# Optimization experiments

Hardware: AMD Instinct MI355X
Metric: run time of the kernel (lower is better)

The kernel has to match this reference:

```python
import jax, jax.numpy as jnp
import numpy as np

SEQ_LEN, N_VARS, N_SKILLS, D_IN = 120, 9, 32, 1
BATCH = 32768


def setup_inputs() -> dict:
    key = jax.random.key(0)
    ks = jax.random.split(key, 8)
    H, D = N_SKILLS, D_IN
    s = 1.0 / np.sqrt(H)  # torch LSTMCell init scale
    return {
        "x": jax.random.normal(ks[0], (BATCH, N_VARS * SEQ_LEN), dtype=jnp.float32),
        # nn.LSTMCell params (gate order i,f,g,o)
        "W_ih": jax.random.uniform(ks[1], (4 * H, D), jnp.float32, -s, s),
        "W_hh": jax.random.uniform(ks[2], (4 * H, H), jnp.float32, -s, s),
        "b_ih": jax.random.uniform(ks[3], (4 * H,), jnp.float32, -s, s),
        "b_hh": jax.random.uniform(ks[4], (4 * H,), jnp.float32, -s, s),
        # contextual gate params: cg_w Linear(D,H,bias=False), cg_u Linear(H,H)
        "cg_w": jax.random.uniform(ks[5], (H, D), jnp.float32, -s, s),
        "cg_u": jax.random.uniform(ks[6], (H, H), jnp.float32, -s, s),
        "cg_b": jax.random.uniform(ks[7], (H,), jnp.float32, -s, s),
    }


def reference(x, W_ih, W_hh, b_ih, b_hh, cg_w, cg_u, cg_b):
    B = x.shape[0]
    H = N_SKILLS
    # [B, V*T] -> fold the 9 independent variable-sequences into the batch dim
    # (the same cell weights are shared across vars), then scan over time.
    xs = x.reshape(B * N_VARS, SEQ_LEN, D_IN)
    xs = jnp.moveaxis(xs, 1, 0)  # [T, B*V, D_IN]

    def step(carry, xt):
        h, c = carry  # each [B*V, H]
        gates = xt @ W_ih.T + b_ih + h @ W_hh.T + b_hh  # [B*V, 4H]
        i, f, g, o = jnp.split(gates, 4, axis=-1)
        i = jax.nn.sigmoid(i)
        f = jax.nn.sigmoid(f)
        g = jnp.tanh(g)
        c_new = f * c + i * g
        # contextual gate uses the *previous* h
        cg = jax.nn.sigmoid(xt @ cg_w.T + h @ cg_u.T + cg_b)
        h_new = cg * jnp.tanh(c_new)
        return (h_new, c_new), None

    zeros = jnp.zeros((B * N_VARS, H), dtype=x.dtype)
    (h, _), _ = jax.lax.scan(step, (zeros, zeros), xs)
    # [B*V, H] -> [B, V*H] (variable-major, matching torch.cat over vars)
    return h.reshape(B, N_VARS * H)
```

## Files before the change

### kernel.cpp

```cpp
#include <hip/hip_runtime.h>


#define NV 9
#define TLEN 120
#define HS 32
#define BATCH_ 32768
#define NSEQ (BATCH_ * NV)
#define NBATCH (NSEQ / 16)
#define WPB 4
#define GRID_ (NBATCH / WPB)

#define TCHUNK 60
#define XSTRIDE 20
#define HSTRIDE 36

#define XT_WORDS   (TCHUNK * XSTRIDE)
#define HB_WORDS   (16 * HSTRIDE)
#define XT_OFF     0
#define HB_OFF     (WPB * XT_WORDS)
#define BLO_OFF    (HB_OFF + WPB * HB_WORDS)
#define POOL_WORDS (BLO_OFF + 8 * 64 * 4)

#define LOG2E 1.4426950408889634f
#define TWOL  2.8853900817779268f

typedef __attribute__((ext_vector_type(8))) short bf16x8;
typedef __attribute__((ext_vector_type(4))) float f32x4;
typedef __attribute__((ext_vector_type(4))) unsigned int u32x4;

__device__ __forceinline__ float fast_exp2(float x) { return __builtin_amdgcn_exp2f(x); }
__device__ __forceinline__ float fast_rcp(float x)  { return __builtin_amdgcn_rcpf(x); }
__device__ __forceinline__ unsigned int fbits(float x) { return __builtin_bit_cast(unsigned int, x); }
__device__ __forceinline__ float bcastf(unsigned int x) { return __builtin_bit_cast(float, x); }

__device__ __forceinline__ f32x4 splat4(float x) { f32x4 v = {x, x, x, x}; return v; }
__device__ __forceinline__ f32x4 fma4(f32x4 a, f32x4 b, f32x4 c) {
  return __builtin_elementwise_fma(a, b, c);
}
__device__ __forceinline__ f32x4 exp24(f32x4 v) {
  f32x4 r;
  r[0] = fast_exp2(v[0]); r[1] = fast_exp2(v[1]);
  r[2] = fast_exp2(v[2]); r[3] = fast_exp2(v[3]);
  return r;
}
__device__ __forceinline__ f32x4 rcp4(f32x4 v) {
  f32x4 r;
  r[0] = fast_rcp(v[0]); r[1] = fast_rcp(v[1]);
  r[2] = fast_rcp(v[2]); r[3] = fast_rcp(v[3]);
  return r;
}

__device__ __forceinline__ void lstm_elem(f32x4 ai, f32x4 af, f32x4 ag, f32x4 ac,
                                          f32x4& ct, f32x4& h) {
  const f32x4 one4 = splat4(1.0f);
  f32x4 Ei = exp24(ai), Ef = exp24(af), Eg = exp24(ag), Ea = exp24(ac);
  f32x4 pi_ = Ei + one4, pf_ = Ef + one4, pg_ = Eg + one4, pa_ = Ea + one4;
  f32x4 u   = fma4(Eg, splat4(TWOL), splat4(-TWOL));
  f32x4 P   = pi_ * pg_;
  f32x4 tt  = pf_ * u;
  f32x4 num = fma4(ct, P, tt);
  f32x4 den = pf_ * P;
  ct = num * rcp4(den);
  f32x4 Ec  = exp24(ct);
  h = (one4 - Ec) * rcp4(pa_ * (Ec + one4));
}

__global__ __launch_bounds__(256, 2) void cglstm_kernel(
    const float* __restrict__ x,
    const float* __restrict__ W_ih,
    const float* __restrict__ W_hh,
    const float* __restrict__ b_ih,
    const float* __restrict__ b_hh,
    const float* __restrict__ cg_w,
    const float* __restrict__ cg_u,
    const float* __restrict__ cg_b,
    float* __restrict__ out)
{
  const int lane = threadIdx.x & 63;
  const int wid  = threadIdx.x >> 6;
  const int col  = lane & 15;
  const int quad = lane >> 4;

  __shared__ __align__(16) unsigned int pool[POOL_WORDS];
  float* __restrict__ xTw = (float*)&pool[XT_OFF + wid * XT_WORDS];
  unsigned int* hb = &pool[HB_OFF + wid * HB_WORDS];
  u32x4* blo_t = (u32x4*)&pool[BLO_OFF];

  bf16x8 bhi[8];
  float wx[8], bb[8];
#pragma unroll
  for (int tile = 0; tile < 8; ++tile) {
    const int n = col + (tile & 1) * 16;
    const float sc_ = ((tile >> 1) == 2) ? -TWOL : -LOG2E;
    const float* wrow = (tile < 6) ? (W_hh + (size_t)((tile >> 1) * HS + n) * HS)
                                   : (cg_u + (size_t)n * HS);
    bf16x8 vh, vl;
#pragma unroll
    for (int e = 0; e < 8; ++e) {
      float wv = wrow[quad * 8 + e] * sc_;
      unsigned int wbits = fbits(wv);
      float lo_f = wv - bcastf(wbits & 0xffff0000u);
      vh[e] = (short)(wbits >> 16);
      vl[e] = (short)(fbits(lo_f) >> 16);
    }
    bhi[tile] = vh;
    blo_t[tile * 64 + lane] = __builtin_bit_cast(u32x4, vl);
    if (tile < 6) {
      const int gg = tile >> 1;
      wx[tile] = W_ih[gg * HS + n] * sc_;
      bb[tile] = (b_ih[gg * HS + n] + b_hh[gg * HS + n]) * sc_;
    } else {
      wx[tile] = cg_w[n] * sc_;
      bb[tile] = cg_b[n] * sc_;
    }
  }

  const int p = blockIdx.x * WPB + wid;
  const float4* xb = (const float4*)(x + (size_t)p * 16 * TLEN);

  for (int i = lane; i < 16 * HSTRIDE; i += 64) hb[i] = 0u;
  f32x4 ct0 = splat4(0.f), ct1 = splat4(0.f), h0 = splat4(0.f), h1 = splat4(0.f);

#pragma unroll 1
  for (int chunk = 0; chunk < 2; ++chunk) {
    for (int i = lane; i < 240; i += 64) {
      int s = i / 15;
      int j = i - s * 15;
      float4 v = xb[s * 30 + chunk * 15 + j];
      int t0 = j * 4;
      xTw[(t0 + 0) * XSTRIDE + s] = v.x;
      xTw[(t0 + 1) * XSTRIDE + s] = v.y;
      xTw[(t0 + 2) * XSTRIDE + s] = v.z;
      xTw[(t0 + 3) * XSTRIDE + s] = v.w;
    }

#pragma unroll 1
    for (int tl = 0; tl < TCHUNK; ++tl) {
      f32x4 xt4 = *(const f32x4*)&xTw[tl * XSTRIDE + quad * 4];
      f32x4 acc[8];
#pragma unroll
      for (int tile = 0; tile < 8; ++tile)
        acc[tile] = fma4(splat4(wx[tile]), xt4, splat4(bb[tile]));
      const unsigned int* hrow = &hb[col * HSTRIDE + quad * 8];
      u32x4 wa = *(const u32x4*)hrow;
      u32x4 wz = *(const u32x4*)(hrow + 4);
      u32x4 hi4, lo4;
      hi4[0] = __builtin_amdgcn_perm(wa[1], wa[0], 0x05040100u);
      hi4[1] = __builtin_amdgcn_perm(wa[3], wa[2], 0x05040100u);
      hi4[2] = __builtin_amdgcn_perm(wz[1], wz[0], 0x05040100u);
      hi4[3] = __builtin_amdgcn_perm(wz[3], wz[2], 0x05040100u);
      lo4[0] = __builtin_amdgcn_perm(wa[1], wa[0], 0x07060302u);
      lo4[1] = __builtin_amdgcn_perm(wa[3], wa[2], 0x07060302u);
      lo4[2] = __builtin_amdgcn_perm(wz[1], wz[0], 0x07060302u);
      lo4[3] = __builtin_amdgcn_perm(wz[3], wz[2], 0x07060302u);
      bf16x8 ahi = __builtin_bit_cast(bf16x8, hi4);
      bf16x8 alo = __builtin_bit_cast(bf16x8, lo4);
#pragma unroll
      for (int tile = 0; tile < 8; ++tile) {
        bf16x8 blo_c = __builtin_bit_cast(bf16x8, blo_t[tile * 64 + lane]);
        acc[tile] = __builtin_amdgcn_mfma_f32_16x16x32_bf16(ahi, bhi[tile], acc[tile], 0, 0, 0);
        acc[tile] = __builtin_amdgcn_mfma_f32_16x16x32_bf16(alo, bhi[tile], acc[tile], 0, 0, 0);
        acc[tile] = __builtin_amdgcn_mfma_f32_16x16x32_bf16(ahi, blo_c, acc[tile], 0, 0, 0);
      }
      lstm_elem(acc[0], acc[2], acc[4], acc[6], ct0, h0);
      lstm_elem(acc[1], acc[3], acc[5], acc[7], ct1, h1);
#pragma unroll
      for (int r = 0; r < 4; ++r) {
        unsigned int hbits = fbits(h0[r]);
        float lof = h0[r] - bcastf(hbits & 0xffff0000u);
        hb[(quad * 4 + r) * HSTRIDE + col] =
            __builtin_amdgcn_perm(fbits(lof), hbits, 0x07060302u);
        unsigned int hbits1 = fbits(h1[r]);
        float lof1 = h1[r] - bcastf(hbits1 & 0xffff0000u);
        hb[(quad * 4 + r) * HSTRIDE + col + 16] =
            __builtin_amdgcn_perm(fbits(lof1), hbits1, 0x07060302u);
      }
    }
  }

  float* ob = out + (size_t)p * 16 * HS;
#pragma unroll
  for (int r = 0; r < 4; ++r) {
    ob[(quad * 4 + r) * HS + col]      = h0[r];
    ob[(quad * 4 + r) * HS + col + 16] = h1[r];
  }
}

extern "C" void kernel_launch(void* const* d_in, const int* in_sizes, int n_in,
                              void* d_out, int out_size, void* d_ws, size_t ws_size,
                              hipStream_t stream) {
  const float* x    = (const float*)d_in[0];
  const float* W_ih = (const float*)d_in[1];
  const float* W_hh = (const float*)d_in[2];
  const float* b_ih = (const float*)d_in[3];
  const float* b_hh = (const float*)d_in[4];
  const float* cg_w = (const float*)d_in[5];
  const float* cg_u = (const float*)d_in[6];
  const float* cg_b = (const float*)d_in[7];
  float* out = (float*)d_out;

  dim3 grid(GRID_), block(256);
  hipLaunchKernelGGL(cglstm_kernel, grid, block, 0, stream,
                     x, W_ih, W_hh, b_ih, b_hh, cg_w, cg_u, cg_b, out);
}
```

Baseline: 1.367 ms.

## Pre-transpose x in a separate kernel and stream timesteps from global memory

Adds a transpose kernel that writes x in time-major order per 16-sequence group to the workspace. The LSTM kernel then prefetches the next timestep's inputs straight from global memory instead of staging chunks through LDS. It also keeps the low bf16 weight halves in registers rather than LDS and groups the MFMAs by pass. This removes the in-kernel LDS transpose and cuts LDS use, in exchange for an extra launch, a full write and re-read of x through the workspace, and higher register pressure. The old path is kept as a fallback for when the workspace is too small.

```diff
diff --git a/kernel.cpp b/kernel.cpp
--- a/kernel.cpp
+++ b/kernel.cpp
@@ -10,16 +10,12 @@
 #define WPB 4
 #define GRID_ (NBATCH / WPB)
 
-#define TCHUNK 60
-#define XSTRIDE 20
 #define HSTRIDE 36
-
-#define XT_WORDS   (TCHUNK * XSTRIDE)
+#define WBSTRIDE 20
+
 #define HB_WORDS   (16 * HSTRIDE)
-#define XT_OFF     0
-#define HB_OFF     (WPB * XT_WORDS)
-#define BLO_OFF    (HB_OFF + WPB * HB_WORDS)
-#define POOL_WORDS (BLO_OFF + 8 * 64 * 4)
+#define WB_OFF     (WPB * HB_WORDS)
+#define POOL_WORDS (WB_OFF + 16 * WBSTRIDE)
 
 #define LOG2E 1.4426950408889634f
 #define TWOL  2.8853900817779268f
@@ -65,8 +61,30 @@
   h = (one4 - Ec) * rcp4(pa_ * (Ec + one4));
 }
 
+__global__ __launch_bounds__(256) void xpose_kernel(
+    const float* __restrict__ x, float* __restrict__ xt) {
+  const int p = blockIdx.x;
+  __shared__ float tile[16 * TLEN];
+  const float4* xb = (const float4*)(x + (size_t)p * 16 * TLEN);
+  float4* ob = (float4*)(xt + (size_t)p * 16 * TLEN);
+  for (int i = threadIdx.x; i < 480; i += 256)
+    ((float4*)tile)[i] = xb[i];
+  __syncthreads();
+  for (int i = threadIdx.x; i < 480; i += 256) {
+    int o0 = i * 4;
+    int t  = o0 >> 4;
+    int e  = o0 & 15;
+    float4 v;
+    v.x = tile[(e + 0) * TLEN + t];
+    v.y = tile[(e + 1) * TLEN + t];
+    v.z = tile[(e + 2) * TLEN + t];
+    v.w = tile[(e + 3) * TLEN + t];
+    ob[i] = v;
+  }
+}
+
 __global__ __launch_bounds__(256, 2) void cglstm_kernel(
-    const float* __restrict__ x,
+    const float* __restrict__ xt_ws,
     const float* __restrict__ W_ih,
     const float* __restrict__ W_hh,
     const float* __restrict__ b_ih,
@@ -82,9 +100,134 @@
   const int quad = lane >> 4;
 
   __shared__ __align__(16) unsigned int pool[POOL_WORDS];
-  float* __restrict__ xTw = (float*)&pool[XT_OFF + wid * XT_WORDS];
-  unsigned int* hb = &pool[HB_OFF + wid * HB_WORDS];
-  u32x4* blo_t = (u32x4*)&pool[BLO_OFF];
+  unsigned int* hb = &pool[wid * HB_WORDS];
+  float* wbt = (float*)&pool[WB_OFF];
+
+  bf16x8 bhi[8], blo[8];
+#pragma unroll
+  for (int tile = 0; tile < 8; ++tile) {
+    const int n = col + (tile & 1) * 16;
+    const float sc_ = ((tile >> 1) == 2) ? -TWOL : -LOG2E;
+    const float* wrow = (tile < 6) ? (W_hh + (size_t)((tile >> 1) * HS + n) * HS)
+                                   : (cg_u + (size_t)n * HS);
+    bf16x8 vh, vl;
+#pragma unroll
+    for (int e = 0; e < 8; ++e) {
+      float wv = wrow[quad * 8 + e] * sc_;
+      unsigned int wbits = fbits(wv);
+      float lo_f = wv - bcastf(wbits & 0xffff0000u);
+      vh[e] = (short)(wbits >> 16);
+      vl[e] = (short)(fbits(lo_f) >> 16);
+    }
+    bhi[tile] = vh; blo[tile] = vl;
+    float wxv, bbv;
+    if (tile < 6) {
+      const int gg = tile >> 1;
+      wxv = W_ih[gg * HS + n] * sc_;
+      bbv = (b_ih[gg * HS + n] + b_hh[gg * HS + n]) * sc_;
+    } else {
+      wxv = cg_w[n] * sc_;
+      bbv = cg_b[n] * sc_;
+    }
+    if (quad == 0) {
+      wbt[col * WBSTRIDE + tile]     = wxv;
+      wbt[col * WBSTRIDE + 8 + tile] = bbv;
+    }
+  }
+
+  const int p = blockIdx.x * WPB + wid;
+  const f32x4* xrow = (const f32x4*)(xt_ws + (size_t)p * 16 * TLEN);
+
+  for (int i = lane; i < HB_WORDS / 4; i += 64) ((u32x4*)hb)[i] = u32x4{0,0,0,0};
+  f32x4 ct0 = splat4(0.f), ct1 = splat4(0.f), h0 = splat4(0.f), h1 = splat4(0.f);
+
+  f32x4 xt_cur = xrow[quad];
+
+#pragma unroll 1
+  for (int t = 0; t < TLEN; ++t) {
+    int tn = (t < TLEN - 1) ? (t + 1) : t;
+    f32x4 xt_nxt = xrow[tn * 4 + quad];
+    f32x4 wx03 = *(const f32x4*)&wbt[col * WBSTRIDE + 0];
+    f32x4 wx47 = *(const f32x4*)&wbt[col * WBSTRIDE + 4];
+    f32x4 bb03 = *(const f32x4*)&wbt[col * WBSTRIDE + 8];
+    f32x4 bb47 = *(const f32x4*)&wbt[col * WBSTRIDE + 12];
+    f32x4 acc[8];
+#pragma unroll
+    for (int k = 0; k < 4; ++k)
+      acc[k] = fma4(splat4(wx03[k]), xt_cur, splat4(bb03[k]));
+#pragma unroll
+    for (int k = 0; k < 4; ++k)
+      acc[4 + k] = fma4(splat4(wx47[k]), xt_cur, splat4(bb47[k]));
+    const unsigned int* hrow = &hb[col * HSTRIDE + quad * 8];
+    u32x4 wa = *(const u32x4*)hrow;
+    u32x4 wz = *(const u32x4*)(hrow + 4);
+    u32x4 hi4, lo4;
+    hi4[0] = __builtin_amdgcn_perm(wa[1], wa[0], 0x05040100u);
+    hi4[1] = __builtin_amdgcn_perm(wa[3], wa[2], 0x05040100u);
+    hi4[2] = __builtin_amdgcn_perm(wz[1], wz[0], 0x05040100u);
+    hi4[3] = __builtin_amdgcn_perm(wz[3], wz[2], 0x05040100u);
+    lo4[0] = __builtin_amdgcn_perm(wa[1], wa[0], 0x07060302u);
+    lo4[1] = __builtin_amdgcn_perm(wa[3], wa[2], 0x07060302u);
+    lo4[2] = __builtin_amdgcn_perm(wz[1], wz[0], 0x07060302u);
+    lo4[3] = __builtin_amdgcn_perm(wz[3], wz[2], 0x07060302u);
+    bf16x8 ahi = __builtin_bit_cast(bf16x8, hi4);
+    bf16x8 alo = __builtin_bit_cast(bf16x8, lo4);
+#pragma unroll
+    for (int k = 0; k < 8; ++k)
+      acc[k] = __builtin_amdgcn_mfma_f32_16x16x32_bf16(ahi, bhi[k], acc[k], 0, 0, 0);
+#pragma unroll
+    for (int k = 0; k < 8; ++k)
+      acc[k] = __builtin_amdgcn_mfma_f32_16x16x32_bf16(alo, bhi[k], acc[k], 0, 0, 0);
+#pragma unroll
+    for (int k = 0; k < 8; ++k)
+      acc[k] = __builtin_amdgcn_mfma_f32_16x16x32_bf16(ahi, blo[k], acc[k], 0, 0, 0);
+    lstm_elem(acc[0], acc[2], acc[4], acc[6], ct0, h0);
+    lstm_elem(acc[1], acc[3], acc[5], acc[7], ct1, h1);
+#pragma unroll
+    for (int r = 0; r < 4; ++r) {
+      unsigned int hbits = fbits(h0[r]);
+      float lof = h0[r] - bcastf(hbits & 0xffff0000u);
+      hb[(quad * 4 + r) * HSTRIDE + col] =
+          __builtin_amdgcn_perm(fbits(lof), hbits, 0x07060302u);
+      unsigned int hbits1 = fbits(h1[r]);
+      float lof1 = h1[r] - bcastf(hbits1 & 0xffff0000u);
+      hb[(quad * 4 + r) * HSTRIDE + col + 16] =
+          __builtin_amdgcn_perm(fbits(lof1), hbits1, 0x07060302u);
+    }
+    xt_cur = xt_nxt;
+  }
+
+  float* ob = out + (size_t)p * 16 * HS;
+#pragma unroll
+  for (int r = 0; r < 4; ++r) {
+    ob[(quad * 4 + r) * HS + col]      = h0[r];
+    ob[(quad * 4 + r) * HS + col + 16] = h1[r];
+  }
+}
+
+#define TCHUNK 60
+#define XSTRIDE 20
+#define FXT_WORDS   (TCHUNK * XSTRIDE)
+#define FHB_OFF     (WPB * FXT_WORDS)
+#define FBLO_OFF    (FHB_OFF + WPB * HB_WORDS)
+#define FPOOL_WORDS (FBLO_OFF + 8 * 64 * 4)
+
+__global__ __launch_bounds__(256, 2) void cglstm_kernel_fb(
+    const float* __restrict__ x,
+    const float* __restrict__ W_ih, const float* __restrict__ W_hh,
+    const float* __restrict__ b_ih, const float* __restrict__ b_hh,
+    const float* __restrict__ cg_w, const float* __restrict__ cg_u,
+    const float* __restrict__ cg_b, float* __restrict__ out)
+{
+  const int lane = threadIdx.x & 63;
+  const int wid  = threadIdx.x >> 6;
+  const int col  = lane & 15;
+  const int quad = lane >> 4;
+
+  __shared__ __align__(16) unsigned int pool[FPOOL_WORDS];
+  float* __restrict__ xTw = (float*)&pool[wid * FXT_WORDS];
+  unsigned int* hb = &pool[FHB_OFF + wid * HB_WORDS];
+  u32x4* blo_t = (u32x4*)&pool[FBLO_OFF];
 
   bf16x8 bhi[8];
   float wx[8], bb[8];
@@ -133,7 +276,6 @@
       xTw[(t0 + 2) * XSTRIDE + s] = v.z;
       xTw[(t0 + 3) * XSTRIDE + s] = v.w;
     }
-
 #pragma unroll 1
     for (int tl = 0; tl < TCHUNK; ++tl) {
       f32x4 xt4 = *(const f32x4*)&xTw[tl * XSTRIDE + quad * 4];
@@ -199,7 +341,14 @@
   const float* cg_b = (const float*)d_in[7];
   float* out = (float*)d_out;
 
-  dim3 grid(GRID_), block(256);
-  hipLaunchKernelGGL(cglstm_kernel, grid, block, 0, stream,
-                     x, W_ih, W_hh, b_ih, b_hh, cg_w, cg_u, cg_b, out);
-}
+  const size_t ws_need = (size_t)NBATCH * 16 * TLEN * sizeof(float);
+  if (d_ws != nullptr && ws_size >= ws_need) {
+    float* xt = (float*)d_ws;
+    hipLaunchKernelGGL(xpose_kernel, dim3(NBATCH), dim3(256), 0, stream, x, xt);
+    hipLaunchKernelGGL(cglstm_kernel, dim3(GRID_), dim3(256), 0, stream,
+                       xt, W_ih, W_hh, b_ih, b_hh, cg_w, cg_u, cg_b, out);
+  } else {
+    hipLaunchKernelGGL(cglstm_kernel_fb, dim3(GRID_), dim3(256), 0, stream,
+                       x, W_ih, W_hh, b_ih, b_hh, cg_w, cg_u, cg_b, out);
+  }
+}
```

Result: slower. 1.426 ms (+4.3%).
